# Performance work log

Measured on AMD Instinct MI355X. Metric: run time of the kernel, lower is better.

The kernel has to match this reference:

```python
import jax, jax.numpy as jnp
import numpy as np


def setup_inputs() -> dict:
    key = jax.random.key(0)
    k1, k2 = jax.random.split(key)
    T, D, K = 100000, 768, 500  # frames, feature dim (HuBERT base), k-means clusters
    feat = jax.random.normal(k1, (T, D), dtype=jnp.float32)
    C = jax.random.normal(k2, (D, K), dtype=jnp.float32)  # cluster centers, transposed as in module
    return {"feat": feat, "C": C}


def reference(feat, C):
    # Squared euclidean distance expanded: ||f||^2 - 2 f.C + ||c||^2
    Cnorm = jnp.sum(C * C, axis=0, keepdims=True)            # [1, K]
    fnorm = jnp.sum(feat * feat, axis=1, keepdims=True)       # [T, 1]
    dist = fnorm - 2.0 * jnp.matmul(feat, C) + Cnorm          # [T, K]
    return jnp.argmin(dist, axis=1)[None, :]                  # [1, T] cluster ids
```

## Files before the change

kernel.cpp:

```cpp
#include <hip/hip_runtime.h>
#include <float.h>

#define D_DIM 768
#define K_DIM 500
#define NDT   24
#define BM    64
#define NTH   256
#define PB_STRIDE 100352

typedef _Float16 f16x8 __attribute__((ext_vector_type(8)));
typedef float    f32x4 __attribute__((ext_vector_type(4)));


__global__ void cnorm_partial_kernel(const float* __restrict__ C,
                                     double* __restrict__ partial, int K) {
    const int k = threadIdx.x;
    const int w = blockIdx.x;
    double s = 0.0;
    if (k < K) {
        const int d0 = w * (D_DIM / 16);
        for (int d = d0; d < d0 + (D_DIM / 16); ++d) {
            const float c = C[(size_t)d * K + k];
            s = fma((double)c, (double)c, s);
        }
    }
    partial[w * 512 + k] = s;
}

__global__ void cnorm_finish_kernel(const double* __restrict__ partial,
                                    float* __restrict__ cnorm, int K) {
    const int k = threadIdx.x;
    if (k < K) {
        double s = 0.0;
        for (int w = 0; w < 16; ++w) s += partial[w * 512 + k];
        cnorm[k] = (float)s;
    } else {
        cnorm[k] = FLT_MAX;
    }
}

__global__ void packB_kernel(const float* __restrict__ C,
                             _Float16* __restrict__ BpH,
                             _Float16* __restrict__ BpL) {
    const int idx = blockIdx.x * 256 + threadIdx.x;
    const int col = idx & 511;
    const int dt  = idx >> 9;
    f16x8 h[4], l[4];
    #pragma unroll
    for (int c = 0; c < 4; ++c)
        #pragma unroll
        for (int j = 0; j < 8; ++j) {
            const int k = c * 8 + j;
            const float v = (col < K_DIM)
                          ? C[(size_t)(dt * 32 + k) * K_DIM + col] : 0.0f;
            const _Float16 hh = (_Float16)v;
            h[c][j] = hh;
            l[c][j] = (_Float16)(v - (float)hh);
        }
    f16x8* dH = (f16x8*)(BpH + ((size_t)dt * 512 + col) * 32);
    f16x8* dL = (f16x8*)(BpL + ((size_t)dt * 512 + col) * 32);
    #pragma unroll
    for (int c = 0; c < 4; ++c) { dH[c] = h[c]; dL[c] = l[c]; }
}

__launch_bounds__(NTH, 3)
__global__ void assign_kernel(const float* __restrict__ feat,
                              const _Float16* __restrict__ BpH,
                              const _Float16* __restrict__ BpL,
                              const float* __restrict__ cnorm,
                              float* __restrict__ pbv,
                              int* __restrict__ pbi,
                              int T) {
    __shared__ __align__(16) _Float16 AsH[2][BM * 32];
    __shared__ __align__(16) _Float16 AsL[2][BM * 32];
    __shared__ float red_v[BM * 4];
    __shared__ int   red_i[BM * 4];

    const int tid  = threadIdx.x;
    const int wn   = tid >> 6;
    const int lane = tid & 63;
    const int l15  = lane & 15;
    const int kg   = lane >> 4;
    const int bid  = blockIdx.x;
    const int half = bid & 1;
    const int R0   = (bid >> 1) * BM;

    const int ar = tid >> 2;
    const int ac = (tid & 3) << 3;
    const bool arow_ok = (R0 + ar) < T;
    const float* fptr = feat + (size_t)(R0 + ar) * D_DIM + ac;
    const int asl = ((ac >> 3) + (ar >> 1)) & 3;

    const int colbase = half * 256 + wn * 64 + l15;
    const _Float16* bpH = BpH + (size_t)colbase * 32 + kg * 8;
    const _Float16* bpL = BpL + (size_t)colbase * 32 + kg * 8;

    f32x4 acc[4][4];
    #pragma unroll
    for (int m = 0; m < 4; ++m)
        #pragma unroll
        for (int n = 0; n < 4; ++n) acc[m][n] = (f32x4){0.f, 0.f, 0.f, 0.f};

#define CVT_STORE(V0, V1, BUF) do {                                            \
    const float fa[8] = {(V0).x, (V0).y, (V0).z, (V0).w,                       \
                         (V1).x, (V1).y, (V1).z, (V1).w};                      \
    f16x8 h, l;                                                                \
    _Pragma("unroll")                                                          \
    for (int j = 0; j < 8; ++j) {                                              \
        const _Float16 hh = (_Float16)fa[j];                                   \
        h[j] = hh; l[j] = (_Float16)(fa[j] - (float)hh);                       \
    }                                                                          \
    ((f16x8*)AsH[BUF])[ar * 4 + asl] = h;                                      \
    ((f16x8*)AsL[BUF])[ar * 4 + asl] = l;                                      \
} while (0)

#define SOFT_BARRIER() do {                                                    \
    asm volatile("s_waitcnt lgkmcnt(0)" ::: "memory");                         \
    __builtin_amdgcn_s_barrier();                                              \
} while (0)

#define BODY(DT, CUR0, CUR1, NXT0, NXT1) do {                                  \
    const int cur = (DT) & 1;                                                  \
         \
        \
    const size_t bo = (size_t)(DT) * 16384;                                    \
    f16x8 bH[4], bL[4];                                                        \
    _Pragma("unroll")                                                          \
    for (int nh = 0; nh < 4; ++nh) {                                           \
        bH[nh] = *(const f16x8*)(bpH + bo + nh * 512);                         \
        bL[nh] = *(const f16x8*)(bpL + bo + nh * 512);                         \
    }                                                                          \
          \
    if ((DT) + 2 < NDT && arow_ok) {                                           \
        const float* p = fptr + ((DT) + 2) * 32;                               \
        NXT0 = *(const float4*)(p);                                            \
        NXT1 = *(const float4*)(p + 4);                                        \
    }                                                                          \
                                            \
    f16x8 aH[4], aL[4];                                                        \
    _Pragma("unroll")                                                          \
    for (int m = 0; m < 4; ++m) {                                              \
        const int row = m * 16 + l15;                                          \
        const int sl  = (kg + (row >> 1)) & 3;                                 \
        aH[m] = ((const f16x8*)AsH[cur])[row * 4 + sl];                        \
        aL[m] = ((const f16x8*)AsL[cur])[row * 4 + sl];                        \
    }                                                                          \
    __builtin_amdgcn_s_setprio(1);                                             \
    _Pragma("unroll")                                                          \
    for (int nh = 0; nh < 4; ++nh)                                             \
        _Pragma("unroll")                                                      \
        for (int m = 0; m < 4; ++m) {                                          \
            f32x4 a = acc[m][nh];                                              \
            a = __builtin_amdgcn_mfma_f32_16x16x32_f16(aH[m], bH[nh], a, 0, 0, 0); \
            a = __builtin_amdgcn_mfma_f32_16x16x32_f16(aL[m], bH[nh], a, 0, 0, 0); \
            a = __builtin_amdgcn_mfma_f32_16x16x32_f16(aH[m], bL[nh], a, 0, 0, 0); \
            acc[m][nh] = a;                                                    \
        }                                                                      \
    __builtin_amdgcn_s_setprio(0);                                             \
      \
    if ((DT) + 1 < NDT) {                                                      \
        CVT_STORE(CUR0, CUR1, cur ^ 1);                                        \
    }                                                                          \
    SOFT_BARRIER();                                                            \
} while (0)

    {
        float4 v0 = make_float4(0.f, 0.f, 0.f, 0.f), v1 = v0;
        if (arow_ok) {
            v0 = *(const float4*)(fptr);
            v1 = *(const float4*)(fptr + 4);
        }
        CVT_STORE(v0, v1, 0);
    }
    float4 pa0 = make_float4(0.f, 0.f, 0.f, 0.f), pa1 = pa0;
    float4 pb0 = pa0, pb1 = pa0;
    if (arow_ok) {
        pa0 = *(const float4*)(fptr + 32);
        pa1 = *(const float4*)(fptr + 36);
    }
    __syncthreads();

    for (int it2 = 0; it2 < NDT; it2 += 2) {
        BODY(it2,     pa0, pa1, pb0, pb1);
        BODY(it2 + 1, pb0, pb1, pa0, pa1);
    }
#undef BODY
#undef SOFT_BARRIER
#undef CVT_STORE

    float cn[4];
    #pragma unroll
    for (int nh = 0; nh < 4; ++nh)
        cn[nh] = cnorm[half * 256 + wn * 64 + nh * 16 + l15];

    #pragma unroll
    for (int m = 0; m < 4; ++m) {
        #pragma unroll
        for (int r = 0; r < 4; ++r) {
            float best = cn[0] - 2.0f * acc[m][0][r];
            int   bi   = colbase;
            #pragma unroll
            for (int nh = 1; nh < 4; ++nh) {
                const int col = colbase + nh * 16;
                const float s = cn[nh] - 2.0f * acc[m][nh][r];
                if (s < best || (s == best && col < bi)) { best = s; bi = col; }
            }
            #pragma unroll
            for (int msk = 1; msk < 16; msk <<= 1) {
                const float ov = __shfl_xor(best, msk, 64);
                const int   oi = __shfl_xor(bi,   msk, 64);
                if (ov < best || (ov == best && oi < bi)) { best = ov; bi = oi; }
            }
            if (l15 == 0) {
                const int rl = m * 16 + kg * 4 + r;
                red_v[rl * 4 + wn] = best;
                red_i[rl * 4 + wn] = bi;
            }
        }
    }
    __syncthreads();

    if (tid < BM) {
        float bv = red_v[tid * 4];
        int   bi = red_i[tid * 4];
        #pragma unroll
        for (int w = 1; w < 4; ++w) {
            const float v = red_v[tid * 4 + w];
            const int   i = red_i[tid * 4 + w];
            if (v < bv || (v == bv && i < bi)) { bv = v; bi = i; }
        }
        const int r = R0 + tid;
        if (r < T) {
            pbv[(size_t)half * PB_STRIDE + r] = bv;
            pbi[(size_t)half * PB_STRIDE + r] = bi;
        }
    }
}

__global__ void combine_kernel(const float* __restrict__ pbv,
                               const int* __restrict__ pbi,
                               int* __restrict__ out, int T) {
    const int r = blockIdx.x * 256 + threadIdx.x;
    if (r < T) {
        const float s0 = pbv[r];
        const int   i0 = pbi[r];
        const float s1 = pbv[PB_STRIDE + r];
        const int   i1 = pbi[PB_STRIDE + r];
        out[r] = (s1 < s0) ? i1 : i0;
    }
}

extern "C" void kernel_launch(void* const* d_in, const int* in_sizes, int n_in,
                              void* d_out, int out_size, void* d_ws, size_t ws_size,
                              hipStream_t stream) {
    const float* feat = (const float*)d_in[0];
    const float* C    = (const float*)d_in[1];
    int* out          = (int*)d_out;
    const int T = in_sizes[0] / D_DIM;
    const int K = in_sizes[1] / D_DIM;

    float*     cnorm   = (float*)d_ws;
    double*    partial = (double*)((char*)d_ws + 4096);
    _Float16*  BpH     = (_Float16*)((char*)d_ws + 131072);
    _Float16*  BpL     = (_Float16*)((char*)d_ws + 917504);
    float*     pbv     = (float*)((char*)d_ws + 1703936);
    int*       pbi     = (int*)((char*)d_ws + 2506752);

    hipLaunchKernelGGL(cnorm_partial_kernel, dim3(16), dim3(512), 0, stream,
                       C, partial, K);
    hipLaunchKernelGGL(cnorm_finish_kernel, dim3(1), dim3(512), 0, stream,
                       partial, cnorm, K);
    hipLaunchKernelGGL(packB_kernel, dim3(48), dim3(256), 0, stream,
                       C, BpH, BpL);

    const int nrb = (T + BM - 1) / BM;
    hipLaunchKernelGGL(assign_kernel, dim3(nrb * 2), dim3(NTH), 0, stream,
                       feat, BpH, BpL, cnorm, pbv, pbi, T);
    hipLaunchKernelGGL(combine_kernel, dim3((T + 255) / 256), dim3(256), 0, stream,
                       pbv, pbi, out, T);
}
```

Before: 265.9 us.

## Split column tile across 8 waves and software-pipeline B fragment loads

```diff
diff --git a/kernel.cpp b/kernel.cpp
--- a/kernel.cpp
+++ b/kernel.cpp
@@ -5,10 +5,11 @@
 #define K_DIM 500
 #define NDT   24
 #define BM    64
-#define NTH   256
+#define NTH   512
 #define PB_STRIDE 100352
 
 typedef _Float16 f16x8 __attribute__((ext_vector_type(8)));
+typedef _Float16 f16x4 __attribute__((ext_vector_type(4)));
 typedef float    f32x4 __attribute__((ext_vector_type(4)));
 
 
@@ -63,7 +64,7 @@
     for (int c = 0; c < 4; ++c) { dH[c] = h[c]; dL[c] = l[c]; }
 }
 
-__launch_bounds__(NTH, 3)
+__launch_bounds__(NTH, 4)
 __global__ void assign_kernel(const float* __restrict__ feat,
                               const _Float16* __restrict__ BpH,
                               const _Float16* __restrict__ BpL,
@@ -73,8 +74,8 @@
                               int T) {
     __shared__ __align__(16) _Float16 AsH[2][BM * 32];
     __shared__ __align__(16) _Float16 AsL[2][BM * 32];
-    __shared__ float red_v[BM * 4];
-    __shared__ int   red_i[BM * 4];
+    __shared__ float red_v[BM * 8];
+    __shared__ int   red_i[BM * 8];
 
     const int tid  = threadIdx.x;
     const int wn   = tid >> 6;
@@ -85,33 +86,33 @@
     const int half = bid & 1;
     const int R0   = (bid >> 1) * BM;
 
-    const int ar = tid >> 2;
-    const int ac = (tid & 3) << 3;
+    const int ar = tid >> 3;
+    const int jj = tid & 7;
     const bool arow_ok = (R0 + ar) < T;
-    const float* fptr = feat + (size_t)(R0 + ar) * D_DIM + ac;
-    const int asl = ((ac >> 3) + (ar >> 1)) & 3;
-
-    const int colbase = half * 256 + wn * 64 + l15;
+    const float* fptr = feat + (size_t)(R0 + ar) * D_DIM + jj * 4;
+    const int aslot = (((jj >> 1) + (ar >> 1)) & 3);
+    const int aoff  = ar * 32 + aslot * 8 + (jj & 1) * 4;
+
+    const int colbase = half * 256 + wn * 32 + l15;
     const _Float16* bpH = BpH + (size_t)colbase * 32 + kg * 8;
     const _Float16* bpL = BpL + (size_t)colbase * 32 + kg * 8;
 
-    f32x4 acc[4][4];
+    f32x4 acc[4][2];
     #pragma unroll
     for (int m = 0; m < 4; ++m)
         #pragma unroll
-        for (int n = 0; n < 4; ++n) acc[m][n] = (f32x4){0.f, 0.f, 0.f, 0.f};
-
-#define CVT_STORE(V0, V1, BUF) do {                                            \
-    const float fa[8] = {(V0).x, (V0).y, (V0).z, (V0).w,                       \
-                         (V1).x, (V1).y, (V1).z, (V1).w};                      \
-    f16x8 h, l;                                                                \
+        for (int n = 0; n < 2; ++n) acc[m][n] = (f32x4){0.f, 0.f, 0.f, 0.f};
+
+#define CVT_STORE(V, BUF) do {                                                 \
+    const float fa_[4] = {(V).x, (V).y, (V).z, (V).w};                         \
+    f16x4 h_, l_;                                                              \
     _Pragma("unroll")                                                          \
-    for (int j = 0; j < 8; ++j) {                                              \
-        const _Float16 hh = (_Float16)fa[j];                                   \
-        h[j] = hh; l[j] = (_Float16)(fa[j] - (float)hh);                       \
-    }                                                                          \
-    ((f16x8*)AsH[BUF])[ar * 4 + asl] = h;                                      \
-    ((f16x8*)AsL[BUF])[ar * 4 + asl] = l;                                      \
+    for (int j = 0; j < 4; ++j) {                                              \
+        const _Float16 hh = (_Float16)fa_[j];                                  \
+        h_[j] = hh; l_[j] = (_Float16)(fa_[j] - (float)hh);                    \
+    }                                                                          \
+    *(f16x4*)(AsH[BUF] + aoff) = h_;                                           \
+    *(f16x4*)(AsL[BUF] + aoff) = l_;                                           \
 } while (0)
 
 #define SOFT_BARRIER() do {                                                    \
@@ -119,22 +120,19 @@
     __builtin_amdgcn_s_barrier();                                              \
 } while (0)
 
-#define BODY(DT, CUR0, CUR1, NXT0, NXT1) do {                                  \
+#define BODY(DT, BCH, BCL, BNH, BNL, ACUR, ANXT) do {                          \
     const int cur = (DT) & 1;                                                  \
-         \
-        \
-    const size_t bo = (size_t)(DT) * 16384;                                    \
-    f16x8 bH[4], bL[4];                                                        \
-    _Pragma("unroll")                                                          \
-    for (int nh = 0; nh < 4; ++nh) {                                           \
-        bH[nh] = *(const f16x8*)(bpH + bo + nh * 512);                         \
-        bL[nh] = *(const f16x8*)(bpL + bo + nh * 512);                         \
-    }                                                                          \
-          \
+           \
+    if ((DT) + 1 < NDT) {                                                      \
+        const size_t bo1 = (size_t)((DT) + 1) * 16384;                         \
+        BNH[0] = *(const f16x8*)(bpH + bo1);                                   \
+        BNH[1] = *(const f16x8*)(bpH + bo1 + 512);                             \
+        BNL[0] = *(const f16x8*)(bpL + bo1);                                   \
+        BNL[1] = *(const f16x8*)(bpL + bo1 + 512);                             \
+    }                                                                          \
+                                                     \
     if ((DT) + 2 < NDT && arow_ok) {                                           \
-        const float* p = fptr + ((DT) + 2) * 32;                               \
-        NXT0 = *(const float4*)(p);                                            \
-        NXT1 = *(const float4*)(p + 4);                                        \
+        ANXT = *(const float4*)(fptr + ((DT) + 2) * 32);                       \
     }                                                                          \
                                             \
     f16x8 aH[4], aL[4];                                                        \
@@ -145,53 +143,52 @@
         aH[m] = ((const f16x8*)AsH[cur])[row * 4 + sl];                        \
         aL[m] = ((const f16x8*)AsL[cur])[row * 4 + sl];                        \
     }                                                                          \
+         \
     __builtin_amdgcn_s_setprio(1);                                             \
     _Pragma("unroll")                                                          \
-    for (int nh = 0; nh < 4; ++nh)                                             \
+    for (int nh = 0; nh < 2; ++nh)                                             \
         _Pragma("unroll")                                                      \
         for (int m = 0; m < 4; ++m) {                                          \
             f32x4 a = acc[m][nh];                                              \
-            a = __builtin_amdgcn_mfma_f32_16x16x32_f16(aH[m], bH[nh], a, 0, 0, 0); \
-            a = __builtin_amdgcn_mfma_f32_16x16x32_f16(aL[m], bH[nh], a, 0, 0, 0); \
-            a = __builtin_amdgcn_mfma_f32_16x16x32_f16(aH[m], bL[nh], a, 0, 0, 0); \
+            a = __builtin_amdgcn_mfma_f32_16x16x32_f16(aH[m], BCH[nh], a, 0, 0, 0); \
+            a = __builtin_amdgcn_mfma_f32_16x16x32_f16(aL[m], BCH[nh], a, 0, 0, 0); \
+            a = __builtin_amdgcn_mfma_f32_16x16x32_f16(aH[m], BCL[nh], a, 0, 0, 0); \
             acc[m][nh] = a;                                                    \
         }                                                                      \
     __builtin_amdgcn_s_setprio(0);                                             \
-      \
+                  \
     if ((DT) + 1 < NDT) {                                                      \
-        CVT_STORE(CUR0, CUR1, cur ^ 1);                                        \
+        CVT_STORE(ACUR, cur ^ 1);                                              \
     }                                                                          \
     SOFT_BARRIER();                                                            \
 } while (0)
 
     {
-        float4 v0 = make_float4(0.f, 0.f, 0.f, 0.f), v1 = v0;
-        if (arow_ok) {
-            v0 = *(const float4*)(fptr);
-            v1 = *(const float4*)(fptr + 4);
-        }
-        CVT_STORE(v0, v1, 0);
-    }
-    float4 pa0 = make_float4(0.f, 0.f, 0.f, 0.f), pa1 = pa0;
-    float4 pb0 = pa0, pb1 = pa0;
-    if (arow_ok) {
-        pa0 = *(const float4*)(fptr + 32);
-        pa1 = *(const float4*)(fptr + 36);
-    }
-    __syncthreads();
+        float4 v = make_float4(0.f, 0.f, 0.f, 0.f);
+        if (arow_ok) v = *(const float4*)(fptr);
+        CVT_STORE(v, 0);
+    }
+    f16x8 bAH[2], bAL[2], bBH[2], bBL[2];
+    bAH[0] = *(const f16x8*)(bpH);
+    bAH[1] = *(const f16x8*)(bpH + 512);
+    bAL[0] = *(const f16x8*)(bpL);
+    bAL[1] = *(const f16x8*)(bpL + 512);
+    float4 avA = make_float4(0.f, 0.f, 0.f, 0.f), avB = avA;
+    if (arow_ok) avA = *(const float4*)(fptr + 32);
+    SOFT_BARRIER();
 
     for (int it2 = 0; it2 < NDT; it2 += 2) {
-        BODY(it2,     pa0, pa1, pb0, pb1);
-        BODY(it2 + 1, pb0, pb1, pa0, pa1);
+        BODY(it2,     bAH, bAL, bBH, bBL, avA, avB);
+        BODY(it2 + 1, bBH, bBL, bAH, bAL, avB, avA);
     }
 #undef BODY
 #undef SOFT_BARRIER
 #undef CVT_STORE
 
-    float cn[4];
-    #pragma unroll
-    for (int nh = 0; nh < 4; ++nh)
-        cn[nh] = cnorm[half * 256 + wn * 64 + nh * 16 + l15];
+    float cn[2];
+    #pragma unroll
+    for (int nh = 0; nh < 2; ++nh)
+        cn[nh] = cnorm[half * 256 + wn * 32 + nh * 16 + l15];
 
     #pragma unroll
     for (int m = 0; m < 4; ++m) {
@@ -199,10 +196,9 @@
         for (int r = 0; r < 4; ++r) {
             float best = cn[0] - 2.0f * acc[m][0][r];
             int   bi   = colbase;
-            #pragma unroll
-            for (int nh = 1; nh < 4; ++nh) {
-                const int col = colbase + nh * 16;
-                const float s = cn[nh] - 2.0f * acc[m][nh][r];
+            {
+                const int col = colbase + 16;
+                const float s = cn[1] - 2.0f * acc[m][1][r];
                 if (s < best || (s == best && col < bi)) { best = s; bi = col; }
             }
             #pragma unroll
@@ -213,20 +209,20 @@
             }
             if (l15 == 0) {
                 const int rl = m * 16 + kg * 4 + r;
-                red_v[rl * 4 + wn] = best;
-                red_i[rl * 4 + wn] = bi;
+                red_v[rl * 8 + wn] = best;
+                red_i[rl * 8 + wn] = bi;
             }
         }
     }
     __syncthreads();
 
     if (tid < BM) {
-        float bv = red_v[tid * 4];
-        int   bi = red_i[tid * 4];
-        #pragma unroll
-        for (int w = 1; w < 4; ++w) {
-            const float v = red_v[tid * 4 + w];
-            const int   i = red_i[tid * 4 + w];
+        float bv = red_v[tid * 8];
+        int   bi = red_i[tid * 8];
+        #pragma unroll
+        for (int w = 1; w < 8; ++w) {
+            const float v = red_v[tid * 8 + w];
+            const int   i = red_i[tid * 8 + w];
             if (v < bv || (v == bv && i < bi)) { bv = v; bi = i; }
         }
         const int r = R0 + tid;
```

New measurement: 297.5 us. 11.9% more time.
